# Optimization experiments

Hardware: AMD Instinct MI355X
Metric: run time of the kernel (lower is better)

## Reference

```python
import jax, jax.numpy as jnp
import numpy as np
from jax import lax


def setup_inputs() -> dict:
    key = jax.random.key(0)
    I = jax.random.uniform(key, (32, 3, 512, 512), dtype=jnp.float32)
    return {"I": I, "k": 15}


def reference(I, k):
    # Channel-wise min -> dark channel (torch does this via -max_pool over transposed channel dim)
    dark = jnp.min(I, axis=1, keepdims=True)  # [B,1,H,W]
    p = k // 2
    # Spatial min-pool kxk, stride 1, pad k//2. torch max_pool2d pads with -inf,
    # so the min-pool equivalent pads with +inf: reduce_window with min and +inf init.
    eroded = lax.reduce_window(
        dark,
        jnp.inf,
        lax.min,
        window_dimensions=(1, 1, k, k),
        window_strides=(1, 1, 1, 1),
        padding=[(0, 0), (0, 0), (p, p), (p, p)],
    )
    return eroded
```

## Files before the change

kernel.cpp:

```cpp
#include <hip/hip_runtime.h>
#include <math.h>

#define BATCH 32
#define CH    3
#define H     512
#define W     512
#define KWIN  15
#define PAD   7
#define TH    8
#define NR    (TH + KWIN - 1)

static __device__ __forceinline__ float2 min2(float2 a, float2 b) {
    float2 r;
    r.x = fminf(a.x, b.x);
    r.y = fminf(a.y, b.y);
    return r;
}

__global__ __launch_bounds__(256, 4) void dcp_fused4(const float* __restrict__ I,
                                                     float* __restrict__ out) {
    const int b  = blockIdx.y;
    const int y0 = blockIdx.x * TH;
    const int t  = threadIdx.x;
    const int x  = t * 2;

    __shared__ float tile[TH][W + 2 * PAD + 2];

    const float* base = I + (size_t)b * CH * H * W;

    float2 v[NR];

    #pragma unroll
    for (int i = 0; i < NR; ++i) {
        const int y = min(max(y0 - PAD + i, 0), H - 1);
        v[i] = *(const float2*)(base + ((size_t)0 * H + y) * W + x);
    }
    #pragma unroll
    for (int i = 0; i < NR; ++i) {
        const int y = min(max(y0 - PAD + i, 0), H - 1);
        v[i] = min2(v[i], *(const float2*)(base + ((size_t)1 * H + y) * W + x));
    }
    #pragma unroll
    for (int i = 0; i < NR; ++i) {
        const int y = min(max(y0 - PAD + i, 0), H - 1);
        v[i] = min2(v[i], *(const float2*)(base + ((size_t)2 * H + y) * W + x));
    }
    if (blockIdx.x == 0 || blockIdx.x == gridDim.x - 1) {
        const float2 inf2 = make_float2(INFINITY, INFINITY);
        #pragma unroll
        for (int i = 0; i < NR; ++i) {
            const int y = y0 - PAD + i;
            if (y < 0 || y >= H) v[i] = inf2;
        }
    }

    float2 P[PAD];
    P[0] = v[15];
    #pragma unroll
    for (int k = 1; k < PAD; ++k) P[k] = min2(P[k - 1], v[15 + k]);
    float2 U = v[14];
    #pragma unroll
    for (int i = 13; i >= 8; --i) U = min2(U, v[i]);
    #pragma unroll
    for (int i = PAD; i >= 0; --i) {
        U = min2(U, v[i]);
        const float2 o = (i > 0) ? min2(U, P[i - 1]) : U;
        *(float2*)&tile[i][PAD + x] = o;
    }

    if (t < PAD) {
        #pragma unroll
        for (int r = 0; r < TH; ++r) tile[r][t] = INFINITY;
    } else if (t < 2 * PAD) {
        #pragma unroll
        for (int r = 0; r < TH; ++r) tile[r][W + t] = INFINITY;
    }
    __syncthreads();

    #pragma unroll
    for (int r = 0; r < TH; ++r) {
        float2 w[8];
        #pragma unroll
        for (int j = 0; j < 8; ++j) w[j] = *(const float2*)&tile[r][x + 2 * j];
        float m = fminf(w[0].y, w[7].x);
        #pragma unroll
        for (int j = 1; j < 7; ++j) m = fminf(m, fminf(w[j].x, w[j].y));
        float2 o;
        o.x = fminf(m, w[0].x);
        o.y = fminf(m, w[7].y);
        *(float2*)(out + ((size_t)b * H + y0 + r) * W + x) = o;
    }
}

extern "C" void kernel_launch(void* const* d_in, const int* in_sizes, int n_in,
                              void* d_out, int out_size, void* d_ws, size_t ws_size,
                              hipStream_t stream) {
    const float* I = (const float*)d_in[0];
    float* out = (float*)d_out;
    dcp_fused4<<<dim3(H / TH, BATCH), dim3(256), 0, stream>>>(I, out);
}
```

Baseline: 198.2 us.

## Split fused dark-channel erosion into horizontal and vertical pass kernels

Replaces the single fused kernel with two launches. The first computes the channel min and horizontal 15-wide min per row into a workspace buffer. The second does the vertical 15-tall min with a van Herk style prefix/suffix scheme over 16-row tiles. This removes the vertical halo re-reads of the 3-channel input, which the fused kernel did for 22 rows per 8 output rows. In exchange it adds a full intermediate write and read through global memory plus a second launch.

```diff
diff --git a/kernel.cpp b/kernel.cpp
--- a/kernel.cpp
+++ b/kernel.cpp
@@ -7,8 +7,7 @@
 #define W     512
 #define KWIN  15
 #define PAD   7
-#define TH    8
-#define NR    (TH + KWIN - 1)
+#define T2    16
 
 static __device__ __forceinline__ float2 min2(float2 a, float2 b) {
     float2 r;
@@ -17,79 +16,86 @@
     return r;
 }
 
-__global__ __launch_bounds__(256, 4) void dcp_fused4(const float* __restrict__ I,
-                                                     float* __restrict__ out) {
-    const int b  = blockIdx.y;
-    const int y0 = blockIdx.x * TH;
+__global__ void dcp_p1(const float* __restrict__ I, float* __restrict__ tmp) {
+    const int bh = blockIdx.x;
+    const int b  = bh >> 9;
+    const int h  = bh & (H - 1);
     const int t  = threadIdx.x;
     const int x  = t * 2;
 
-    __shared__ float tile[TH][W + 2 * PAD + 2];
+    __shared__ float s[W + 2 * PAD + 2];
 
-    const float* base = I + (size_t)b * CH * H * W;
-
-    float2 v[NR];
-
-    #pragma unroll
-    for (int i = 0; i < NR; ++i) {
-        const int y = min(max(y0 - PAD + i, 0), H - 1);
-        v[i] = *(const float2*)(base + ((size_t)0 * H + y) * W + x);
-    }
-    #pragma unroll
-    for (int i = 0; i < NR; ++i) {
-        const int y = min(max(y0 - PAD + i, 0), H - 1);
-        v[i] = min2(v[i], *(const float2*)(base + ((size_t)1 * H + y) * W + x));
-    }
-    #pragma unroll
-    for (int i = 0; i < NR; ++i) {
-        const int y = min(max(y0 - PAD + i, 0), H - 1);
-        v[i] = min2(v[i], *(const float2*)(base + ((size_t)2 * H + y) * W + x));
-    }
-    if (blockIdx.x == 0 || blockIdx.x == gridDim.x - 1) {
-        const float2 inf2 = make_float2(INFINITY, INFINITY);
-        #pragma unroll
-        for (int i = 0; i < NR; ++i) {
-            const int y = y0 - PAD + i;
-            if (y < 0 || y >= H) v[i] = inf2;
-        }
-    }
-
-    float2 P[PAD];
-    P[0] = v[15];
-    #pragma unroll
-    for (int k = 1; k < PAD; ++k) P[k] = min2(P[k - 1], v[15 + k]);
-    float2 U = v[14];
-    #pragma unroll
-    for (int i = 13; i >= 8; --i) U = min2(U, v[i]);
-    #pragma unroll
-    for (int i = PAD; i >= 0; --i) {
-        U = min2(U, v[i]);
-        const float2 o = (i > 0) ? min2(U, P[i - 1]) : U;
-        *(float2*)&tile[i][PAD + x] = o;
-    }
-
+    const float* p = I + ((size_t)b * CH * H + h) * W + x;
+    const float2 a0 = *(const float2*)(p);
+    const float2 a1 = *(const float2*)(p + (size_t)H * W);
+    const float2 a2 = *(const float2*)(p + (size_t)2 * H * W);
+    const float2 d  = min2(min2(a0, a1), a2);
+    s[PAD + x]     = d.x;
+    s[PAD + x + 1] = d.y;
     if (t < PAD) {
-        #pragma unroll
-        for (int r = 0; r < TH; ++r) tile[r][t] = INFINITY;
-    } else if (t < 2 * PAD) {
-        #pragma unroll
-        for (int r = 0; r < TH; ++r) tile[r][W + t] = INFINITY;
+        s[t]           = INFINITY;
+        s[PAD + W + t] = INFINITY;
     }
     __syncthreads();
 
+    float2 w[8];
     #pragma unroll
-    for (int r = 0; r < TH; ++r) {
-        float2 w[8];
+    for (int j = 0; j < 8; ++j) w[j] = *(const float2*)&s[x + 2 * j];
+    float m = fminf(w[0].y, w[7].x);
+    #pragma unroll
+    for (int j = 1; j < 7; ++j) m = fminf(m, fminf(w[j].x, w[j].y));
+    float2 o;
+    o.x = fminf(m, w[0].x);
+    o.y = fminf(m, w[7].y);
+    *(float2*)(tmp + ((size_t)b * H + h) * W + x) = o;
+}
+
+__global__ void dcp_p2(const float* __restrict__ tmp, float* __restrict__ out) {
+    const int x  = threadIdx.x * 2;
+    const int y0 = blockIdx.x * T2;
+    const int b  = blockIdx.y;
+
+    const float* col = tmp + (size_t)b * H * W + x;
+    float*       o   = out + (size_t)b * H * W + x;
+
+    float2 vb[KWIN];
+    #pragma unroll
+    for (int j = 0; j < KWIN; ++j) {
+        const int y = min(y0 + 8 + j, H - 1);
+        vb[j] = *(const float2*)(col + (size_t)y * W);
+    }
+    if (y0 + 8 + KWIN - 1 >= H) {
+        const float2 inf2 = make_float2(INFINITY, INFINITY);
         #pragma unroll
-        for (int j = 0; j < 8; ++j) w[j] = *(const float2*)&tile[r][x + 2 * j];
-        float m = fminf(w[0].y, w[7].x);
+        for (int j = 0; j < KWIN; ++j)
+            if (y0 + 8 + j >= H) vb[j] = inf2;
+    }
+    float2 P[KWIN];
+    P[0] = vb[0];
+    #pragma unroll
+    for (int j = 1; j < KWIN; ++j) P[j] = min2(P[j - 1], vb[j]);
+    *(float2*)(o + (size_t)(y0 + 15) * W) = P[14];
+
+    float2 va[KWIN];
+    #pragma unroll
+    for (int i = 0; i < KWIN; ++i) {
+        const int y = max(y0 - PAD + i, 0);
+        va[i] = *(const float2*)(col + (size_t)y * W);
+    }
+    if (y0 == 0) {
+        const float2 inf2 = make_float2(INFINITY, INFINITY);
         #pragma unroll
-        for (int j = 1; j < 7; ++j) m = fminf(m, fminf(w[j].x, w[j].y));
-        float2 o;
-        o.x = fminf(m, w[0].x);
-        o.y = fminf(m, w[7].y);
-        *(float2*)(out + ((size_t)b * H + y0 + r) * W + x) = o;
+        for (int i = 0; i < PAD; ++i) va[i] = inf2;
     }
+    float2 run = va[14];
+    *(float2*)(o + (size_t)(y0 + 14) * W) = min2(run, P[13]);
+    #pragma unroll
+    for (int r = 13; r >= 1; --r) {
+        run = min2(run, va[r]);
+        *(float2*)(o + (size_t)(y0 + r) * W) = min2(run, P[r - 1]);
+    }
+    run = min2(run, va[0]);
+    *(float2*)(o + (size_t)y0 * W) = run;
 }
 
 extern "C" void kernel_launch(void* const* d_in, const int* in_sizes, int n_in,
@@ -97,5 +103,8 @@
                               hipStream_t stream) {
     const float* I = (const float*)d_in[0];
     float* out = (float*)d_out;
-    dcp_fused4<<<dim3(H / TH, BATCH), dim3(256), 0, stream>>>(I, out);
+    float* tmp = (float*)d_ws;
+
+    dcp_p1<<<dim3(BATCH * H), dim3(256), 0, stream>>>(I, tmp);
+    dcp_p2<<<dim3(H / T2, BATCH), dim3(256), 0, stream>>>(tmp, out);
 }
```

After: 166.4 us. -16.0%, faster.
